# Optimization experiments

Measured on AMD Instinct MI355X. Metric: run time of the kernel, lower is better.

## Reference

```python
import jax, jax.numpy as jnp
import numpy as np

T, N, E = 336, 3233, 20000
FEAT, D, H = 14, 64, 128


def setup_inputs() -> dict:
    key = jax.random.key(0)
    ks = jax.random.split(key, 12)
    s = lambda k, shape, fan: jax.random.normal(k, shape, jnp.float32) / np.sqrt(fan)
    return {
        "x": jax.random.normal(ks[0], (T, N, FEAT), jnp.float32),
        "edge_index": jax.random.randint(ks[1], (2, E), 0, N, jnp.int64 if jax.config.jax_enable_x64 else jnp.int32),
        "edge_weight": jax.random.uniform(ks[2], (E,), jnp.float32),
        "W1": s(ks[3], (FEAT, D), FEAT), "b1": jnp.zeros((D,), jnp.float32),
        "W2": s(ks[4], (D, D), D), "b2": jnp.zeros((D,), jnp.float32),
        "county_bias": s(ks[5], (N, D), D),
        "W_ih": s(ks[6], (4 * H, D), D), "W_hh": s(ks[7], (4 * H, H), H),
        "b_ih": jnp.zeros((4 * H,), jnp.float32), "b_hh": jnp.zeros((4 * H,), jnp.float32),
        "Wm1": s(ks[8], (H, H // 2), H), "bm1": jnp.zeros((H // 2,), jnp.float32),
        "Wm2": s(ks[9], (H // 2, 1), H // 2), "bm2": jnp.zeros((1,), jnp.float32),
    }


def _gcn_norm(edge_index, edge_weight, n):
    # PyG GCNConv: add self-loops (weight 1) + symmetric normalization
    loop = jnp.arange(n, dtype=edge_index.dtype)
    src = jnp.concatenate([edge_index[0], loop])
    dst = jnp.concatenate([edge_index[1], loop])
    w = jnp.concatenate([edge_weight, jnp.ones((n,), edge_weight.dtype)])
    deg = jax.ops.segment_sum(w, dst, num_segments=n)
    dis = jnp.where(deg > 0, jax.lax.rsqrt(jnp.where(deg > 0, deg, 1.0)), 0.0)
    return src, dst, dis[src] * w * dis[dst]


def _gcn(h, src, dst, norm, W, b):
    # h: [T,N,Fin] -> [T,N,Fout]; transform then gather-scale-scatter over edges
    hw = jnp.einsum("tnf,fd->tnd", h, W)
    msg = hw[:, src, :] * norm[None, :, None]          # [T,E',Fout]
    out = jnp.zeros_like(hw).at[:, dst, :].add(msg)
    return out + b


def reference(x, edge_index, edge_weight, W1, b1, W2, b2, county_bias,
              W_ih, W_hh, b_ih, b_hh, Wm1, bm1, Wm2, bm2):
    n = x.shape[1]
    src, dst, norm = _gcn_norm(edge_index, edge_weight, n)
    h = jax.nn.relu(_gcn(x, src, dst, norm, W1, b1))
    embeds = _gcn(h, src, dst, norm, W2, b2) + county_bias[None]  # [T,N,D]

    hid = W_hh.shape[1]
    def step(carry, x_t):  # x_t: [N,D]
        hprev, cprev = carry
        g = x_t @ W_ih.T + hprev @ W_hh.T + (b_ih + b_hh)
        i, f, gg, o = jnp.split(g, 4, axis=-1)
        c = jax.nn.sigmoid(f) * cprev + jax.nn.sigmoid(i) * jnp.tanh(gg)
        hh = jax.nn.sigmoid(o) * jnp.tanh(c)
        return (hh, c), None

    init = (jnp.zeros((n, hid), x.dtype), jnp.zeros((n, hid), x.dtype))
    (h_final, _), _ = jax.lax.scan(step, init, embeds)
    z = jax.nn.relu(h_final @ Wm1 + bm1)
    return (z @ Wm2 + bm2)[:, 0]
```

## Files before the change

### kernel.cpp

```cpp
#include <hip/hip_runtime.h>
#include <math.h>


#define T_DIM 336
#define N_DIM 3233
#define E_DIM 20000
#define FEAT  14
#define D_DIM 64
#define H_DIM 128
#define ET    (E_DIM + N_DIM)

typedef _Float16 f16;
typedef _Float16 half8_t __attribute__((ext_vector_type(8)));
typedef float float4_t __attribute__((ext_vector_type(4)));

__device__ __forceinline__ float sigf(float x) {
    return __builtin_amdgcn_rcpf(1.f + exp2f(-1.4426950408889634f * x));
}
__device__ __forceinline__ float tanhfast(float x) {
    return 1.f - 2.f * __builtin_amdgcn_rcpf(1.f + exp2f(2.8853900817779268f * x));
}


__global__ void k_init(int* cnt, int* fill) {
    int i = blockIdx.x * 256 + threadIdx.x;
    if (i < N_DIM) { cnt[i] = 0; fill[i] = 0; }
}

__global__ void k_cnt(const int* __restrict__ ei, int* cnt) {
    int e = blockIdx.x * 256 + threadIdx.x;
    if (e < E_DIM) atomicAdd(&cnt[ei[E_DIM + e]], 1);
}

__global__ void k_scan(const int* __restrict__ cnt, int* __restrict__ rowp) {
    __shared__ int csum[1024];
    int tid = threadIdx.x;
    int base = tid * 4;
    int v[4];
    int s = 0;
    #pragma unroll
    for (int m = 0; m < 4; m++) {
        int idx = base + m;
        int len = (idx < N_DIM) ? (cnt[idx] + 1) : 0;
        v[m] = s; s += len;
    }
    csum[tid] = s;
    __syncthreads();
    for (int off = 1; off < 1024; off <<= 1) {
        int t2 = (tid >= off) ? csum[tid - off] : 0;
        __syncthreads();
        csum[tid] += t2;
        __syncthreads();
    }
    int pre = (tid > 0) ? csum[tid - 1] : 0;
    #pragma unroll
    for (int m = 0; m < 4; m++) {
        int idx = base + m;
        if (idx <= N_DIM) rowp[idx] = pre + v[m];
    }
}

__global__ void k_fill(const int* __restrict__ ei, const int* __restrict__ rowp,
                       int* fill, int* __restrict__ eid) {
    int e = blockIdx.x * 256 + threadIdx.x;
    if (e < ET) {
        int d = (e < E_DIM) ? ei[E_DIM + e] : (e - E_DIM);
        int p = rowp[d] + atomicAdd(&fill[d], 1);
        eid[p] = e;
    }
}

__global__ void k_sortdeg(const float* __restrict__ ew, const int* __restrict__ rowp,
                          int* __restrict__ eid, float* __restrict__ dis) {
    int n = blockIdx.x * 256 + threadIdx.x;
    if (n >= N_DIM) return;
    int p0 = rowp[n], p1 = rowp[n + 1];
    for (int i = p0 + 1; i < p1; i++) {
        int key = eid[i];
        int j = i - 1;
        while (j >= p0 && eid[j] > key) { eid[j + 1] = eid[j]; j--; }
        eid[j + 1] = key;
    }
    float deg = 0.f;
    for (int p = p0; p < p1; p++) {
        int e = eid[p];
        deg += (e < E_DIM) ? ew[e] : 1.0f;
    }
    dis[n] = rsqrtf(deg);
}

__global__ void k_csrmat(const int* __restrict__ ei, const float* __restrict__ ew,
                         const float* __restrict__ dis, const int* __restrict__ rowp,
                         const int* __restrict__ eid, int* __restrict__ csrc,
                         float* __restrict__ cnrm) {
    int n = blockIdx.x * 256 + threadIdx.x;
    if (n >= N_DIM) return;
    float dn = dis[n];
    int p0 = rowp[n], p1 = rowp[n + 1];
    for (int p = p0; p < p1; p++) {
        int e = eid[p];
        int s; float w;
        if (e < E_DIM) { s = ei[e]; w = ew[e]; }
        else           { s = e - E_DIM; w = 1.0f; }
        csrc[p] = s;
        cnrm[p] = dis[s] * w * dn;
    }
}

__global__ void k_wprep(const float* __restrict__ W2, const float* __restrict__ Wih,
                        const float* __restrict__ Whh, f16* __restrict__ wfbuf) {
    int idx = blockIdx.x * 256 + threadIdx.x;
    if (idx >= 8 * 4 * 6 * 64) return;
    int lane = idx & 63;
    int ks = (idx >> 6) % 6;
    int ct = ((idx >> 6) / 6) & 3;
    int wv = (idx >> 6) / 24;
    int q = lane >> 4, r = lane & 15;
    int g = 128 * ct + 16 * wv + r;
    f16* dst = wfbuf + (long)idx * 8;
    if (ks < 2) {
        const float* wir = Wih + (long)g * 64;
        #pragma unroll
        for (int j = 0; j < 8; j++) {
            int k = 32 * ks + 8 * q + j;
            const float* w2r = W2 + (long)k * 64;
            float s = 0.f;
            #pragma unroll 16
            for (int d = 0; d < 64; d++) s += w2r[d] * wir[d];
            dst[j] = (f16)s;
        }
    } else {
        const float* src = Whh + (long)g * 128 + 32 * (ks - 2) + 8 * q;
        #pragma unroll
        for (int j = 0; j < 8; j++) dst[j] = (f16)src[j];
    }
}

__global__ void k_gbias(const float* __restrict__ county, const float* __restrict__ b2,
                        const float* __restrict__ Wih, const float* __restrict__ bih,
                        const float* __restrict__ bhh, float* __restrict__ gbias) {
    long id = (long)blockIdx.x * 256 + threadIdx.x;
    if (id >= (long)N_DIM * 512) return;
    int n = (int)(id >> 9), g = (int)(id & 511);
    const float* wir = Wih + (long)g * 64;
    const float* cn = county + (long)n * 64;
    float s = bih[g] + bhh[g];
    #pragma unroll 16
    for (int d = 0; d < 64; d++) s += (b2[d] + cn[d]) * wir[d];
    gbias[id] = s;
}

__global__ void k_gcn1(const float* __restrict__ x, const int* __restrict__ rowp,
                       const int* __restrict__ csrc, const float* __restrict__ cnrm,
                       const float* __restrict__ W1, const float* __restrict__ b1,
                       f16* __restrict__ h, int tc) {
    __shared__ float g1[4][4][16];
    int lane = threadIdx.x & 63;
    int wv = threadIdx.x >> 6;
    long wid = ((long)blockIdx.x * 256 + threadIdx.x) >> 6;
    int ntg = (tc + 3) >> 2;
    bool wlive = wid < (long)N_DIM * ntg;

    int n = 0, tg = 0;
    if (wlive) { n = (int)(wid % N_DIM); tg = (int)(wid / N_DIM); }
    int j = lane >> 4, d = lane & 15;
    int tj = 4 * tg + j;
    bool live = wlive && (d < FEAT) && (tj < tc);

    float acc = 0.f;
    if (wlive) {
        int p0 = rowp[n], p1 = rowp[n + 1];
        for (int p = p0; p < p1; p++) {
            int s = csrc[p];
            float w = cnrm[p];
            if (live) acc += w * x[((long)tj * N_DIM + s) * FEAT + d];
        }
    }
    g1[wv][j][d] = acc;
    __syncthreads();

    if (!wlive) return;
    float wc[FEAT];
    #pragma unroll
    for (int k = 0; k < FEAT; k++) wc[k] = W1[k * 64 + lane];
    float bb = b1[lane];
    #pragma unroll
    for (int jj = 0; jj < 4; jj++) {
        int tjj = 4 * tg + jj;
        if (tjj >= tc) break;
        float a = bb;
        #pragma unroll
        for (int k = 0; k < FEAT; k++) a += g1[wv][jj][k] * wc[k];
        h[((long)tjj * N_DIM + n) * 64 + lane] = (f16)fmaxf(a, 0.f);
    }
}

__global__ void k_agg2(const f16* __restrict__ h, const int* __restrict__ rowp,
                       const int* __restrict__ csrc, const float* __restrict__ cnrm,
                       f16* __restrict__ ah, int tc) {
    int lane = threadIdx.x & 63;
    long wid = ((long)blockIdx.x * 256 + threadIdx.x) >> 6;
    int ntg = (tc + 3) >> 2;
    if (wid >= (long)N_DIM * ntg) return;
    int n = (int)(wid % N_DIM);
    int tg = (int)(wid / N_DIM);
    int tbase = 4 * tg;
    float acc0 = 0.f, acc1 = 0.f, acc2 = 0.f, acc3 = 0.f;
    int p0 = rowp[n], p1 = rowp[n + 1];
    for (int p = p0; p < p1; p++) {
        int s = csrc[p];
        float w = cnrm[p];
        const f16* base = h + ((long)tbase * N_DIM + s) * 64 + lane;
        acc0 += w * (float)base[0];
        if (tbase + 1 < tc) acc1 += w * (float)base[(long)N_DIM * 64];
        if (tbase + 2 < tc) acc2 += w * (float)base[(long)N_DIM * 128];
        if (tbase + 3 < tc) acc3 += w * (float)base[(long)N_DIM * 192];
    }
    f16* dst = ah + ((long)tbase * N_DIM + n) * 64 + lane;
    dst[0] = (f16)acc0;
    if (tbase + 1 < tc) dst[(long)N_DIM * 64] = (f16)acc1;
    if (tbase + 2 < tc) dst[(long)N_DIM * 128] = (f16)acc2;
    if (tbase + 3 < tc) dst[(long)N_DIM * 192] = (f16)acc3;
}

__global__ __attribute__((amdgpu_flat_work_group_size(512, 512), amdgpu_waves_per_eu(2, 2)))
void k_lstm(
    const f16* __restrict__ ah, const f16* __restrict__ wfbuf,
    const float* __restrict__ gbias,
    const float* __restrict__ Wm1, const float* __restrict__ bm1,
    const float* __restrict__ Wm2, const float* __restrict__ bm2,
    float* __restrict__ Hst, float* __restrict__ Cst,
    int tc, int do_init, int do_head, float* __restrict__ out) {
    __shared__ __align__(16) f16   xh[2][16][136];
    __shared__ __align__(16) float hd[16][132];
    __shared__ __align__(16) float zs[16][64];

    int tid = threadIdx.x;
    int wv = tid >> 6, lane = tid & 63, q = lane >> 4, r = lane & 15;
    int nb = blockIdx.x * 16;
    int cnt = min(16, N_DIM - nb);
    int u = 16 * wv + r;

    float4_t wfr[4][6];
    #pragma unroll
    for (int ct = 0; ct < 4; ct++)
        #pragma unroll
        for (int ks = 0; ks < 6; ks++)
            wfr[ct][ks] = *(const float4_t*)&wfbuf[(long)((((wv * 4 + ct) * 6 + ks) << 6) + lane) * 8];
    #pragma unroll
    for (int ct = 0; ct < 4; ct++)
        #pragma unroll
        for (int ks = 0; ks < 6; ks++)
            asm volatile("" : "+v"(wfr[ct][ks]));

    float gb[4][4];
    #pragma unroll
    for (int reg = 0; reg < 4; reg++) {
        int node = 4 * q + reg;
        int gn = nb + node; if (gn >= N_DIM) gn = N_DIM - 1;
        #pragma unroll
        for (int ct = 0; ct < 4; ct++)
            gb[ct][reg] = gbias[(long)gn * 512 + 128 * ct + u];
    }
    #pragma unroll
    for (int ct = 0; ct < 4; ct++)
        #pragma unroll
        for (int reg = 0; reg < 4; reg++)
            asm volatile("" : "+v"(gb[ct][reg]));

    float cv[4], hvv[4];
    #pragma unroll
    for (int reg = 0; reg < 4; reg++) {
        int node = 4 * q + reg;
        bool live = (!do_init) && (node < cnt);
        hvv[reg] = live ? Hst[(long)(nb + node) * H_DIM + u] : 0.f;
        cv[reg]  = live ? Cst[(long)(nb + node) * H_DIM + u] : 0.f;
        xh[0][node][u] = (f16)hvv[reg];
    }

    int xrow = nb + r; if (xrow >= N_DIM) xrow = N_DIM - 1;
    half8_t xa = *(const half8_t*)(ah + (long)xrow * 64 + 8 * q);
    half8_t xb = *(const half8_t*)(ah + (long)xrow * 64 + 32 + 8 * q);

    int buf = 0;
    __syncthreads();

    for (int t = 0; t < tc; t++) {
        half8_t a2 = *(const half8_t*)&xh[buf][r][8 * q];
        half8_t a3 = *(const half8_t*)&xh[buf][r][32 + 8 * q];
        half8_t a4 = *(const half8_t*)&xh[buf][r][64 + 8 * q];
        half8_t a5 = *(const half8_t*)&xh[buf][r][96 + 8 * q];

        float4_t acc[4];
        #pragma unroll
        for (int ct = 0; ct < 4; ct++) {
            acc[ct][0] = gb[ct][0]; acc[ct][1] = gb[ct][1];
            acc[ct][2] = gb[ct][2]; acc[ct][3] = gb[ct][3];
        }
        #pragma unroll
        for (int ct = 0; ct < 4; ct++)
            acc[ct] = __builtin_amdgcn_mfma_f32_16x16x32_f16(xa, __builtin_bit_cast(half8_t, wfr[ct][0]), acc[ct], 0, 0, 0);
        #pragma unroll
        for (int ct = 0; ct < 4; ct++)
            acc[ct] = __builtin_amdgcn_mfma_f32_16x16x32_f16(xb, __builtin_bit_cast(half8_t, wfr[ct][1]), acc[ct], 0, 0, 0);

        int tn = (t + 1 < tc) ? t + 1 : t;
        const f16* xp = ah + ((long)tn * N_DIM + xrow) * 64;
        xa = *(const half8_t*)(xp + 8 * q);
        xb = *(const half8_t*)(xp + 32 + 8 * q);

        #pragma unroll
        for (int ct = 0; ct < 4; ct++)
            acc[ct] = __builtin_amdgcn_mfma_f32_16x16x32_f16(a2, __builtin_bit_cast(half8_t, wfr[ct][2]), acc[ct], 0, 0, 0);
        #pragma unroll
        for (int ct = 0; ct < 4; ct++)
            acc[ct] = __builtin_amdgcn_mfma_f32_16x16x32_f16(a3, __builtin_bit_cast(half8_t, wfr[ct][3]), acc[ct], 0, 0, 0);
        #pragma unroll
        for (int ct = 0; ct < 4; ct++)
            acc[ct] = __builtin_amdgcn_mfma_f32_16x16x32_f16(a4, __builtin_bit_cast(half8_t, wfr[ct][4]), acc[ct], 0, 0, 0);
        #pragma unroll
        for (int ct = 0; ct < 4; ct++)
            acc[ct] = __builtin_amdgcn_mfma_f32_16x16x32_f16(a5, __builtin_bit_cast(half8_t, wfr[ct][5]), acc[ct], 0, 0, 0);

        #pragma unroll
        for (int reg = 0; reg < 4; reg++) {
            float gi = acc[0][reg], gf = acc[1][reg], gg = acc[2][reg], go = acc[3][reg];
            float c = sigf(gf) * cv[reg] + sigf(gi) * tanhfast(gg);
            float hh = sigf(go) * tanhfast(c);
            cv[reg] = c; hvv[reg] = hh;
            xh[buf ^ 1][4 * q + reg][u] = (f16)hh;
        }
        __syncthreads();
        buf ^= 1;
    }

    #pragma unroll
    for (int reg = 0; reg < 4; reg++) {
        int node = 4 * q + reg;
        if (node < cnt) {
            Hst[(long)(nb + node) * H_DIM + u] = hvv[reg];
            Cst[(long)(nb + node) * H_DIM + u] = cv[reg];
        }
    }
    if (!do_head) return;

    #pragma unroll
    for (int reg = 0; reg < 4; reg++) hd[4 * q + reg][u] = hvv[reg];
    __syncthreads();

    for (int i = tid; i < 16 * 64; i += 512) {
        int n = i >> 6, m = i & 63;
        float a = bm1[m];
        #pragma unroll 8
        for (int k = 0; k < H_DIM; k++) a += hd[n][k] * Wm1[k * 64 + m];
        zs[n][m] = fmaxf(a, 0.f);
    }
    __syncthreads();
    if (tid < cnt) {
        float a = bm2[0];
        #pragma unroll 8
        for (int m = 0; m < 64; m++) a += zs[tid][m] * Wm2[m];
        out[nb + tid] = a;
    }
}


extern "C" void kernel_launch(void* const* d_in, const int* in_sizes, int n_in,
                              void* d_out, int out_size, void* d_ws, size_t ws_size,
                              hipStream_t stream) {
    const float* x   = (const float*)d_in[0];
    const int*   ei  = (const int*)d_in[1];
    const float* ew  = (const float*)d_in[2];
    const float* W1  = (const float*)d_in[3];
    const float* b1  = (const float*)d_in[4];
    const float* W2  = (const float*)d_in[5];
    const float* b2  = (const float*)d_in[6];
    const float* cb  = (const float*)d_in[7];
    const float* Wih = (const float*)d_in[8];
    const float* Whh = (const float*)d_in[9];
    const float* bih = (const float*)d_in[10];
    const float* bhh = (const float*)d_in[11];
    const float* Wm1 = (const float*)d_in[12];
    const float* bm1 = (const float*)d_in[13];
    const float* Wm2 = (const float*)d_in[14];
    const float* bm2 = (const float*)d_in[15];
    float* out = (float*)d_out;
    (void)in_sizes; (void)n_in; (void)out_size;

    char* ws = (char*)d_ws;
    size_t off = 0;
    auto alloc = [&](size_t bytes) -> char* {
        char* p = ws + off;
        off = (off + bytes + 255) & ~(size_t)255;
        return p;
    };
    float* dis   = (float*)alloc(N_DIM * 4);
    int*   cnt   = (int*)alloc(N_DIM * 4);
    int*   fill  = (int*)alloc(N_DIM * 4);
    int*   rowp  = (int*)alloc((N_DIM + 1) * 4);
    int*   eid   = (int*)alloc(ET * 4);
    int*   csrc  = (int*)alloc(ET * 4);
    float* cnrm  = (float*)alloc(ET * 4);
    float* Hst   = (float*)alloc((size_t)N_DIM * H_DIM * 4);
    float* Cst   = (float*)alloc((size_t)N_DIM * H_DIM * 4);
    f16*   wfbuf = (f16*)alloc((size_t)8 * 4 * 6 * 64 * 8 * 2);
    float* gbias = (float*)alloc((size_t)N_DIM * 512 * 4);

    const int cand[] = {336, 168, 112, 84, 56, 48, 28, 16, 8, 4};
    int Tc = 4;
    for (int i = 0; i < 10; i++) {
        size_t need = off + (size_t)cand[i] * N_DIM * 256 + 4096;
        if (need <= ws_size) { Tc = cand[i]; break; }
    }
    long rows = (long)Tc * N_DIM;
    f16* hbuf  = (f16*)alloc(rows * 128);
    f16* ahbuf = (f16*)alloc(rows * 128);

    k_init<<<(N_DIM + 255) / 256, 256, 0, stream>>>(cnt, fill);
    k_cnt<<<(E_DIM + 255) / 256, 256, 0, stream>>>(ei, cnt);
    k_scan<<<1, 1024, 0, stream>>>(cnt, rowp);
    k_fill<<<(ET + 255) / 256, 256, 0, stream>>>(ei, rowp, fill, eid);
    k_sortdeg<<<(N_DIM + 255) / 256, 256, 0, stream>>>(ew, rowp, eid, dis);
    k_csrmat<<<(N_DIM + 255) / 256, 256, 0, stream>>>(ei, ew, dis, rowp, eid, csrc, cnrm);
    k_wprep<<<48, 256, 0, stream>>>(W2, Wih, Whh, wfbuf);
    k_gbias<<<(int)(((long)N_DIM * 512 + 255) / 256), 256, 0, stream>>>(cb, b2, Wih, bih, bhh, gbias);

    int ntg = (Tc + 3) >> 2;
    long aggWaves = (long)N_DIM * ntg;
    int aggBlocks = (int)((aggWaves + 3) / 4);
    int lblocks   = (N_DIM + 15) / 16;
    int nChunks   = T_DIM / Tc;

    for (int c = 0; c < nChunks; c++) {
        long t0 = (long)c * Tc;
        k_gcn1<<<aggBlocks, 256, 0, stream>>>(x + t0 * N_DIM * FEAT, rowp, csrc, cnrm,
                                              W1, b1, hbuf, Tc);
        k_agg2<<<aggBlocks, 256, 0, stream>>>(hbuf, rowp, csrc, cnrm, ahbuf, Tc);
        k_lstm<<<lblocks, 512, 0, stream>>>(ahbuf, wfbuf, gbias, Wm1, bm1, Wm2, bm2,
                                            Hst, Cst, Tc, c == 0 ? 1 : 0,
                                            c == nChunks - 1 ? 1 : 0, out);
    }
}
```

Before: 1.161 ms.

## Sub-chunk GCN stages for cache residency and widen agg2 to 8 timesteps

The GCN layer-1 output buffer is split into smaller sub-chunks (Th timesteps), so each h sub-buffer is more likely to stay cache-resident while agg2 gathers from it, while the LSTM still consumes a larger Tc chunk. k_agg2 now processes 8 timesteps per wave instead of 4, reusing each edge's index and weight load across more gathers. The cost is more kernel launches, fewer waves in agg2, and more registers per thread.

New measurement: 1.242 ms. 1.07x slower.

```diff
diff --git a/kernel.cpp b/kernel.cpp
--- a/kernel.cpp
+++ b/kernel.cpp
@@ -200,27 +200,28 @@
                        f16* __restrict__ ah, int tc) {
     int lane = threadIdx.x & 63;
     long wid = ((long)blockIdx.x * 256 + threadIdx.x) >> 6;
-    int ntg = (tc + 3) >> 2;
+    int ntg = (tc + 7) >> 3;
     if (wid >= (long)N_DIM * ntg) return;
     int n = (int)(wid % N_DIM);
     int tg = (int)(wid / N_DIM);
-    int tbase = 4 * tg;
-    float acc0 = 0.f, acc1 = 0.f, acc2 = 0.f, acc3 = 0.f;
+    int tb = 8 * tg;
+    int nt = min(8, tc - tb);
+    float acc[8];
+    #pragma unroll
+    for (int j = 0; j < 8; j++) acc[j] = 0.f;
     int p0 = rowp[n], p1 = rowp[n + 1];
     for (int p = p0; p < p1; p++) {
         int s = csrc[p];
         float w = cnrm[p];
-        const f16* base = h + ((long)tbase * N_DIM + s) * 64 + lane;
-        acc0 += w * (float)base[0];
-        if (tbase + 1 < tc) acc1 += w * (float)base[(long)N_DIM * 64];
-        if (tbase + 2 < tc) acc2 += w * (float)base[(long)N_DIM * 128];
-        if (tbase + 3 < tc) acc3 += w * (float)base[(long)N_DIM * 192];
-    }
-    f16* dst = ah + ((long)tbase * N_DIM + n) * 64 + lane;
-    dst[0] = (f16)acc0;
-    if (tbase + 1 < tc) dst[(long)N_DIM * 64] = (f16)acc1;
-    if (tbase + 2 < tc) dst[(long)N_DIM * 128] = (f16)acc2;
-    if (tbase + 3 < tc) dst[(long)N_DIM * 192] = (f16)acc3;
+        const f16* base = h + ((long)tb * N_DIM + s) * 64 + lane;
+        #pragma unroll
+        for (int j = 0; j < 8; j++)
+            if (j < nt) acc[j] += w * (float)base[(long)j * N_DIM * 64];
+    }
+    f16* dst = ah + ((long)tb * N_DIM + n) * 64 + lane;
+    #pragma unroll
+    for (int j = 0; j < 8; j++)
+        if (j < nt) dst[(long)j * N_DIM * 64] = (f16)acc[j];
 }
 
 __global__ __attribute__((amdgpu_flat_work_group_size(512, 512), amdgpu_waves_per_eu(2, 2)))
@@ -406,15 +407,16 @@
     f16*   wfbuf = (f16*)alloc((size_t)8 * 4 * 6 * 64 * 8 * 2);
     float* gbias = (float*)alloc((size_t)N_DIM * 512 * 4);
 
-    const int cand[] = {336, 168, 112, 84, 56, 48, 28, 16, 8, 4};
-    int Tc = 4;
-    for (int i = 0; i < 10; i++) {
-        size_t need = off + (size_t)cand[i] * N_DIM * 256 + 4096;
-        if (need <= ws_size) { Tc = cand[i]; break; }
-    }
-    long rows = (long)Tc * N_DIM;
-    f16* hbuf  = (f16*)alloc(rows * 128);
-    f16* ahbuf = (f16*)alloc(rows * 128);
+    const int optTc[] = {168, 168, 168, 84, 84, 56, 28, 8, 4};
+    const int optTh[] = { 84,  56,  28, 84, 42, 56, 28, 8, 4};
+    int Tc = 4, Th = 4;
+    for (int i = 0; i < 9; i++) {
+        size_t need = off + (size_t)optTc[i] * N_DIM * 128
+                          + (size_t)optTh[i] * N_DIM * 128 + 4096;
+        if (need <= ws_size) { Tc = optTc[i]; Th = optTh[i]; break; }
+    }
+    f16* ahbuf = (f16*)alloc((size_t)Tc * N_DIM * 128);
+    f16* hbuf  = (f16*)alloc((size_t)Th * N_DIM * 128);
 
     k_init<<<(N_DIM + 255) / 256, 256, 0, stream>>>(cnt, fill);
     k_cnt<<<(E_DIM + 255) / 256, 256, 0, stream>>>(ei, cnt);
@@ -425,17 +427,22 @@
     k_wprep<<<48, 256, 0, stream>>>(W2, Wih, Whh, wfbuf);
     k_gbias<<<(int)(((long)N_DIM * 512 + 255) / 256), 256, 0, stream>>>(cb, b2, Wih, bih, bhh, gbias);
 
-    int ntg = (Tc + 3) >> 2;
-    long aggWaves = (long)N_DIM * ntg;
-    int aggBlocks = (int)((aggWaves + 3) / 4);
-    int lblocks   = (N_DIM + 15) / 16;
-    int nChunks   = T_DIM / Tc;
+    int ntg4 = (Th + 3) >> 2;
+    int ntg8 = (Th + 7) >> 3;
+    int g1Blocks = (int)(((long)N_DIM * ntg4 + 3) / 4);
+    int a2Blocks = (int)(((long)N_DIM * ntg8 + 3) / 4);
+    int lblocks  = (N_DIM + 15) / 16;
+    int nChunks  = T_DIM / Tc;
+    int nSub     = Tc / Th;
 
     for (int c = 0; c < nChunks; c++) {
-        long t0 = (long)c * Tc;
-        k_gcn1<<<aggBlocks, 256, 0, stream>>>(x + t0 * N_DIM * FEAT, rowp, csrc, cnrm,
-                                              W1, b1, hbuf, Tc);
-        k_agg2<<<aggBlocks, 256, 0, stream>>>(hbuf, rowp, csrc, cnrm, ahbuf, Tc);
+        for (int s = 0; s < nSub; s++) {
+            long t0 = (long)c * Tc + (long)s * Th;
+            k_gcn1<<<g1Blocks, 256, 0, stream>>>(x + t0 * N_DIM * FEAT, rowp, csrc, cnrm,
+                                                 W1, b1, hbuf, Th);
+            k_agg2<<<a2Blocks, 256, 0, stream>>>(hbuf, rowp, csrc, cnrm,
+                                                 ahbuf + (long)s * Th * N_DIM * 64, Th);
+        }
         k_lstm<<<lblocks, 512, 0, stream>>>(ahbuf, wfbuf, gbias, Wm1, bm1, Wm2, bm2,
                                             Hst, Cst, Tc, c == 0 ? 1 : 0,
                                             c == nChunks - 1 ? 1 : 0, out);
```
